# Kernel optimization log

Hardware: AMD Instinct MI355X
Metric: run time of the kernel (lower is better)

Reference implementation:

```python
import jax, jax.numpy as jnp
import numpy as np

N = 50000      # nodes
E = 250000     # edges
D = 256        # in_channels
MSG = 256      # msg_dim
TD = 64        # time encoder out_channels
ED = MSG + TD  # edge_dim = 320
H = 4          # heads
C = 64         # out_channels // heads


def setup_inputs() -> dict:
    key = jax.random.key(0)
    ks = jax.random.split(key, 16)
    s_d = 1.0 / np.sqrt(D)
    s_e = 1.0 / np.sqrt(ED)
    return {
        "x": jax.random.normal(ks[0], (N, D), jnp.float32),
        "last_update": jax.random.uniform(ks[1], (N,), jnp.float32) * 1000.0,
        "t": jax.random.uniform(ks[2], (E,), jnp.float32) * 1000.0,
        "msg": jax.random.normal(ks[3], (E, MSG), jnp.float32),
        "edge_index": jax.random.randint(ks[4], (2, E), 0, N, jnp.int32),
        # TimeEncoder: Linear(1, TD) followed by cos
        "time_w": jax.random.normal(ks[5], (TD,), jnp.float32),
        "time_b": jax.random.normal(ks[6], (TD,), jnp.float32) * 0.1,
        # TransformerConv linears (weights stored [out, in] like torch)
        "Wq": jax.random.normal(ks[7], (H * C, D), jnp.float32) * s_d,
        "bq": jnp.zeros((H * C,), jnp.float32),
        "Wk": jax.random.normal(ks[8], (H * C, D), jnp.float32) * s_d,
        "bk": jnp.zeros((H * C,), jnp.float32),
        "Wv": jax.random.normal(ks[9], (H * C, D), jnp.float32) * s_d,
        "bv": jnp.zeros((H * C,), jnp.float32),
        "We": jax.random.normal(ks[10], (H * C, ED), jnp.float32) * s_e,  # lin_edge, no bias
        "Wskip": jax.random.normal(ks[11], (H * C, D), jnp.float32) * s_d,
        "bskip": jnp.zeros((H * C,), jnp.float32),
    }


def reference(x, last_update, t, msg, edge_index, time_w, time_b,
              Wq, bq, Wk, bk, Wv, bv, We, Wskip, bskip):
    src = edge_index[0]  # j: message source
    dst = edge_index[1]  # i: message target

    # time encoding: cos(Linear(1, TD)(rel_t))
    rel_t = last_update[src] - t                              # [E]
    rel_t_enc = jnp.cos(rel_t[:, None] * time_w[None, :] + time_b)  # [E, TD]
    edge_attr = jnp.concatenate([rel_t_enc, msg], axis=-1)    # [E, ED]

    # TransformerConv (heads=4, concat=True, root_weight=True, beta=False, eval mode)
    q = (x @ Wq.T + bq).reshape(N, H, C)
    k = (x @ Wk.T + bk).reshape(N, H, C)
    v = (x @ Wv.T + bv).reshape(N, H, C)
    e = (edge_attr @ We.T).reshape(E, H, C)

    k_j = k[src] + e                                           # [E, H, C]
    alpha = jnp.einsum('ehc,ehc->eh', q[dst], k_j) / np.sqrt(C)  # [E, H]

    # segment softmax over incoming edges of each target node
    m = jax.ops.segment_max(alpha, dst, num_segments=N)        # [N, H]
    m = jnp.where(jnp.isfinite(m), m, 0.0)
    ex = jnp.exp(alpha - m[dst])                               # [E, H]
    denom = jax.ops.segment_sum(ex, dst, num_segments=N)       # [N, H]
    alpha = ex / (denom[dst] + 1e-16)                          # [E, H]

    out_e = (v[src] + e) * alpha[:, :, None]                   # [E, H, C]
    out = jax.ops.segment_sum(out_e, dst, num_segments=N)      # [N, H, C]
    out = out.reshape(N, H * C) + (x @ Wskip.T + bskip)        # skip connection
    return out
```

## Files before the change

kernel.cpp:

```cpp
#include <hip/hip_runtime.h>
#include <math.h>

#define NN 50000
#define EE 250000

typedef float f32x4 __attribute__((ext_vector_type(4)));
typedef __bf16 bf16x8 __attribute__((ext_vector_type(8)));

static __device__ __forceinline__ ushort f2b(float f) {
    __bf16 h = (__bf16)f;
    return *(ushort*)&h;
}
static __device__ __forceinline__ float b2f(ushort u) {
    return __uint_as_float(((unsigned)u) << 16);
}

__global__ void k_prep_w(const float* __restrict__ Wq, const float* __restrict__ bq,
                         const float* __restrict__ Wk, const float* __restrict__ bk,
                         const float* __restrict__ Wv, const float* __restrict__ bv,
                         const float* __restrict__ Wskip, const float* __restrict__ bskip,
                         const float* __restrict__ We,
                         ushort* __restrict__ Wnb, ushort* __restrict__ Web,
                         float* __restrict__ bcat) {
    int i = blockIdx.x * 256 + threadIdx.x;
    int st = gridDim.x * 256;
    for (int idx = i; idx < 1024 * 256; idx += st) {
        int n = idx >> 8, kk = idx & 255;
        int sel = n >> 8, o = n & 255;
        const float* W = (sel == 0) ? Wq : (sel == 1) ? Wk : (sel == 2) ? Wv : Wskip;
        Wnb[idx] = f2b(W[o * 256 + kk]);
    }
    for (int idx = i; idx < 256 * 320; idx += st) Web[idx] = f2b(We[idx]);
    for (int idx = i; idx < 1024; idx += st) {
        int sel = idx >> 8, o = idx & 255;
        const float* b = (sel == 0) ? bq : (sel == 1) ? bk : (sel == 2) ? bv : bskip;
        bcat[idx] = b[o];
    }
}

__global__ void k_zero(unsigned* __restrict__ deg) {
    int i = blockIdx.x * 256 + threadIdx.x;
    if (i < NN) deg[i] = 0u;
}

__global__ void k_hist(const int* __restrict__ ei, unsigned* __restrict__ deg) {
    int i = blockIdx.x * 256 + threadIdx.x;
    if (i < EE) atomicAdd(&deg[ei[EE + i]], 1u);
}

__global__ __launch_bounds__(1024) void k_scan(const unsigned* __restrict__ deg,
                                               unsigned* __restrict__ offs,
                                               unsigned* __restrict__ cursor) {
    __shared__ unsigned part[1024];
    int t = threadIdx.x;
    const int CH = (NN + 1023) / 1024;
    int b0 = t * CH;
    unsigned s = 0;
    for (int i = 0; i < CH; ++i) { int idx = b0 + i; if (idx < NN) s += deg[idx]; }
    part[t] = s;
    __syncthreads();
    for (int d = 1; d < 1024; d <<= 1) {
        unsigned v = (t >= d) ? part[t - d] : 0u;
        __syncthreads();
        part[t] += v;
        __syncthreads();
    }
    unsigned run = (t == 0) ? 0u : part[t - 1];
    for (int i = 0; i < CH; ++i) {
        int idx = b0 + i;
        if (idx < NN) { offs[idx] = run; cursor[idx] = run; run += deg[idx]; }
    }
    if (t == 1023) offs[NN] = EE;
}

__global__ void k_scatter(const int* __restrict__ ei, unsigned* __restrict__ cursor,
                          int* __restrict__ rank) {
    int i = blockIdx.x * 256 + threadIdx.x;
    if (i < EE) {
        unsigned p = atomicAdd(&cursor[ei[EE + i]], 1u);
        rank[i] = (int)p;
    }
}

__global__ __launch_bounds__(256) void k_node_mfma(
        const float* __restrict__ x, const ushort* __restrict__ Wnb,
        const float* __restrict__ bcat,
        ushort* __restrict__ qb, ushort* __restrict__ kb, ushort* __restrict__ vb,
        float* __restrict__ out) {
    __shared__ ushort As[128 * 64];
    __shared__ ushort Bs[128 * 64];
    int tid = threadIdx.x;
    int lane = tid & 63, wid = tid >> 6;
    int wr = wid >> 1, wc = wid & 1;
    int li = lane & 15, g = lane >> 4;
    int bm = blockIdx.x, bn = blockIdx.y;
    f32x4 acc[4][4] = {};
    for (int k0 = 0; k0 < 256; k0 += 64) {
        __syncthreads();
        #pragma unroll
        for (int i = 0; i < 4; ++i) {
            int ch = tid + i * 256;
            int r = ch >> 3, c = ch & 7;
            int row = bm * 128 + r;
            union { ushort u[8]; uint4 v; } s;
            if (row < NN) {
                const float* xr = x + (size_t)row * 256 + k0 + c * 8;
                float4 a = *(const float4*)xr;
                float4 b = *(const float4*)(xr + 4);
                s.u[0] = f2b(a.x); s.u[1] = f2b(a.y); s.u[2] = f2b(a.z); s.u[3] = f2b(a.w);
                s.u[4] = f2b(b.x); s.u[5] = f2b(b.y); s.u[6] = f2b(b.z); s.u[7] = f2b(b.w);
            } else {
                s.v = make_uint4(0, 0, 0, 0);
            }
            *(uint4*)&As[r * 64 + ((c ^ (r & 7)) * 8)] = s.v;
            uint4 vb4 = *(const uint4*)(Wnb + (size_t)(bn * 128 + r) * 256 + k0 + c * 8);
            *(uint4*)&Bs[r * 64 + ((c ^ (r & 7)) * 8)] = vb4;
        }
        __syncthreads();
        #pragma unroll
        for (int kk = 0; kk < 2; ++kk) {
            bf16x8 a[4], b[4];
            #pragma unroll
            for (int m = 0; m < 4; ++m) {
                int r = wr * 64 + m * 16 + li;
                a[m] = *(const bf16x8*)&As[r * 64 + (((kk * 4 + g) ^ (r & 7)) * 8)];
            }
            #pragma unroll
            for (int n = 0; n < 4; ++n) {
                int r = wc * 64 + n * 16 + li;
                b[n] = *(const bf16x8*)&Bs[r * 64 + (((kk * 4 + g) ^ (r & 7)) * 8)];
            }
            #pragma unroll
            for (int m = 0; m < 4; ++m)
                #pragma unroll
                for (int n = 0; n < 4; ++n)
                    acc[m][n] = __builtin_amdgcn_mfma_f32_16x16x32_bf16(a[m], b[n], acc[m][n], 0, 0, 0);
        }
    }
    int sel = bn >> 1;
    int cbase = (bn & 1) * 128;
    ushort* dstb = (sel == 0) ? qb : (sel == 1) ? kb : vb;
    #pragma unroll
    for (int m = 0; m < 4; ++m) {
        #pragma unroll
        for (int r = 0; r < 4; ++r) {
            int row = bm * 128 + wr * 64 + m * 16 + g * 4 + r;
            if (row >= NN) continue;
            #pragma unroll
            for (int n = 0; n < 4; ++n) {
                int coll = wc * 64 + n * 16 + li;
                float val = acc[m][n][r] + bcat[bn * 128 + coll];
                int cin = cbase + coll;
                if (sel < 3) dstb[(size_t)row * 256 + cin] = f2b(val);
                else         out[(size_t)row * 256 + cin] = val;
            }
        }
    }
}

__global__ __launch_bounds__(256) void k_edge_mfma(
        const float* __restrict__ msg, const float* __restrict__ t_arr,
        const float* __restrict__ lu, const float* __restrict__ tw,
        const float* __restrict__ tb, const ushort* __restrict__ Web,
        const ushort* __restrict__ qb, const ushort* __restrict__ kb,
        const ushort* __restrict__ vb, const int* __restrict__ ei,
        const int* __restrict__ rank,
        ushort* __restrict__ ebuf, float* __restrict__ alpha) {
    __shared__ ushort SS[64 * 328];
    __shared__ int s_src[64], s_dst[64], s_rank[64];
    __shared__ float s_relt[64];
    int tid = threadIdx.x;
    int lane = tid & 63, wid = tid >> 6;
    int wr = wid >> 1, wc = wid & 1;
    int li = lane & 15, g = lane >> 4;
    int e0 = blockIdx.x * 64;
    if (tid < 64) {
        int e = e0 + tid;
        if (e >= EE) e = EE - 1;
        int s = ei[e];
        s_src[tid] = s;
        s_dst[tid] = ei[EE + e];
        s_rank[tid] = rank[e];
        s_relt[tid] = lu[s] - t_arr[e];
    }
    f32x4 acc[2][8] = {};
    for (int k0 = 0; k0 < 320; k0 += 64) {
        __syncthreads();
        #pragma unroll
        for (int i = 0; i < 2; ++i) {
            int ch = tid + i * 256;
            int r = ch >> 3, c = ch & 7;
            union { ushort u[8]; uint4 v; } s;
            if (k0 == 0) {
                float rt = s_relt[r];
                #pragma unroll
                for (int j = 0; j < 8; ++j)
                    s.u[j] = f2b(cosf(rt * tw[c * 8 + j] + tb[c * 8 + j]));
            } else {
                int erow = e0 + r; if (erow >= EE) erow = EE - 1;
                const float* mrow = msg + (size_t)erow * 256 + (k0 - 64) + c * 8;
                float4 a = *(const float4*)mrow;
                float4 b = *(const float4*)(mrow + 4);
                s.u[0] = f2b(a.x); s.u[1] = f2b(a.y); s.u[2] = f2b(a.z); s.u[3] = f2b(a.w);
                s.u[4] = f2b(b.x); s.u[5] = f2b(b.y); s.u[6] = f2b(b.z); s.u[7] = f2b(b.w);
            }
            *(uint4*)&SS[r * 64 + ((c ^ (r & 7)) * 8)] = s.v;
        }
        #pragma unroll
        for (int i = 0; i < 8; ++i) {
            int ch = tid + i * 256;
            int r = ch >> 3, c = ch & 7;
            uint4 vb4 = *(const uint4*)(Web + (size_t)r * 320 + k0 + c * 8);
            *(uint4*)&SS[4096 + r * 64 + ((c ^ (r & 7)) * 8)] = vb4;
        }
        __syncthreads();
        #pragma unroll
        for (int kk = 0; kk < 2; ++kk) {
            bf16x8 a[2], b[8];
            #pragma unroll
            for (int m = 0; m < 2; ++m) {
                int r = wr * 32 + m * 16 + li;
                a[m] = *(const bf16x8*)&SS[r * 64 + (((kk * 4 + g) ^ (r & 7)) * 8)];
            }
            #pragma unroll
            for (int n = 0; n < 8; ++n) {
                int r = wc * 128 + n * 16 + li;
                b[n] = *(const bf16x8*)&SS[4096 + r * 64 + (((kk * 4 + g) ^ (r & 7)) * 8)];
            }
            #pragma unroll
            for (int m = 0; m < 2; ++m)
                #pragma unroll
                for (int n = 0; n < 8; ++n)
                    acc[m][n] = __builtin_amdgcn_mfma_f32_16x16x32_bf16(a[m], b[n], acc[m][n], 0, 0, 0);
        }
    }
    __syncthreads();
    #pragma unroll
    for (int i = 0; i < 8; ++i) {
        int idx = tid + i * 256;
        int r = idx >> 5, c = idx & 31;
        uint4 vv = *(const uint4*)(vb + (size_t)s_src[r] * 256 + c * 8);
        *(uint4*)&SS[r * 328 + c * 8] = vv;
    }
    __syncthreads();
    #pragma unroll
    for (int m = 0; m < 2; ++m) {
        #pragma unroll
        for (int r = 0; r < 4; ++r) {
            int el = wr * 32 + m * 16 + g * 4 + r;
            int edge = e0 + el;
            if (edge >= EE) continue;
            size_t rb = (size_t)s_rank[el] * 256;
            #pragma unroll
            for (int n = 0; n < 8; ++n) {
                int col = wc * 128 + n * 16 + li;
                ebuf[rb + col] = f2b(acc[m][n][r] + b2f(SS[el * 328 + col]));
            }
        }
    }
    __syncthreads();
    #pragma unroll
    for (int i = 0; i < 8; ++i) {
        int idx = tid + i * 256;
        int r = idx >> 5, c = idx & 31;
        uint4 kv = *(const uint4*)(kb + (size_t)s_src[r] * 256 + c * 8);
        *(uint4*)&SS[r * 328 + c * 8] = kv;
    }
    __syncthreads();
    #pragma unroll
    for (int m = 0; m < 2; ++m)
        #pragma unroll
        for (int r = 0; r < 4; ++r) {
            int el = wr * 32 + m * 16 + g * 4 + r;
            #pragma unroll
            for (int n = 0; n < 8; ++n)
                acc[m][n][r] += b2f(SS[el * 328 + wc * 128 + n * 16 + li]);
        }
    __syncthreads();
    #pragma unroll
    for (int i = 0; i < 8; ++i) {
        int idx = tid + i * 256;
        int r = idx >> 5, c = idx & 31;
        uint4 qv = *(const uint4*)(qb + (size_t)s_dst[r] * 256 + c * 8);
        *(uint4*)&SS[r * 328 + c * 8] = qv;
    }
    __syncthreads();
    #pragma unroll
    for (int m = 0; m < 2; ++m) {
        #pragma unroll
        for (int r = 0; r < 4; ++r) {
            int el = wr * 32 + m * 16 + g * 4 + r;
            int edge = e0 + el;
            float p0 = 0.f, p1 = 0.f;
            #pragma unroll
            for (int n = 0; n < 8; ++n) {
                float qv = b2f(SS[el * 328 + wc * 128 + n * 16 + li]);
                float tt = qv * acc[m][n][r];
                if (n < 4) p0 += tt; else p1 += tt;
            }
            #pragma unroll
            for (int msk = 1; msk < 16; msk <<= 1) {
                p0 += __shfl_xor(p0, msk);
                p1 += __shfl_xor(p1, msk);
            }
            if (li < 2 && edge < EE) {
                float av = ((li == 0) ? p0 : p1) * 0.125f;
                int h = wc * 2 + li;
                alpha[(size_t)s_rank[el] * 4 + h] = av;
            }
        }
    }
}

__global__ __launch_bounds__(256) void k_gather(
        const ushort* __restrict__ ebuf, const float* __restrict__ alpha,
        const unsigned* __restrict__ offs, float* __restrict__ out) {
    int wid = threadIdx.x >> 6, lane = threadIdx.x & 63;
    int n = blockIdx.x * 4 + wid;
    if (n >= NN) return;
    unsigned p0 = offs[n], p1 = offs[n + 1];
    if (p0 == p1) return;
    int h = lane >> 4;
    int c0 = lane * 4;
    float m = -INFINITY;
    for (unsigned p = p0; p < p1; ++p)
        m = fmaxf(m, alpha[(size_t)p * 4 + h]);
    f32x4 acc = {0.f, 0.f, 0.f, 0.f};
    float denom = 0.f;
    for (unsigned p = p0; p < p1; ++p) {
        float ex = __expf(alpha[(size_t)p * 4 + h] - m);
        ushort4 ev = *(const ushort4*)(ebuf + (size_t)p * 256 + c0);
        acc[0] += b2f(ev.x) * ex;
        acc[1] += b2f(ev.y) * ex;
        acc[2] += b2f(ev.z) * ex;
        acc[3] += b2f(ev.w) * ex;
        denom += ex;
    }
    float inv = 1.f / (denom + 1e-16f);
    float4 o = *(float4*)(out + (size_t)n * 256 + c0);
    o.x += acc[0] * inv;
    o.y += acc[1] * inv;
    o.z += acc[2] * inv;
    o.w += acc[3] * inv;
    *(float4*)(out + (size_t)n * 256 + c0) = o;
}

extern "C" void kernel_launch(void* const* d_in, const int* in_sizes, int n_in,
                              void* d_out, int out_size, void* d_ws, size_t ws_size,
                              hipStream_t stream) {
    const float* x        = (const float*)d_in[0];
    const float* last_upd = (const float*)d_in[1];
    const float* t_arr    = (const float*)d_in[2];
    const float* msg      = (const float*)d_in[3];
    const int*   ei       = (const int*)d_in[4];
    const float* time_w   = (const float*)d_in[5];
    const float* time_b   = (const float*)d_in[6];
    const float* Wq = (const float*)d_in[7];  const float* bq = (const float*)d_in[8];
    const float* Wk = (const float*)d_in[9];  const float* bk = (const float*)d_in[10];
    const float* Wv = (const float*)d_in[11]; const float* bv = (const float*)d_in[12];
    const float* We = (const float*)d_in[13];
    const float* Wsk = (const float*)d_in[14]; const float* bsk = (const float*)d_in[15];
    float* out = (float*)d_out;
    char* base = (char*)d_ws;

    size_t off = 0;
    auto carve = [&](size_t bytes) {
        void* p = base + off;
        off += (bytes + 255) & ~(size_t)255;
        return p;
    };
    ushort* Wnb   = (ushort*)carve((size_t)1024 * 256 * 2);
    ushort* Web   = (ushort*)carve((size_t)256 * 320 * 2);
    float*  bcat  = (float*) carve(1024 * 4);
    ushort* qb    = (ushort*)carve((size_t)NN * 256 * 2);
    ushort* kb    = (ushort*)carve((size_t)NN * 256 * 2);
    ushort* vb    = (ushort*)carve((size_t)NN * 256 * 2);
    ushort* ebuf  = (ushort*)carve((size_t)EE * 256 * 2);
    float*  alpha = (float*) carve((size_t)EE * 4 * 4);
    unsigned* deg    = (unsigned*)carve((size_t)NN * 4);
    unsigned* cursor = (unsigned*)carve((size_t)NN * 4);
    unsigned* offs   = (unsigned*)carve((size_t)(NN + 1) * 4);
    int*      rank   = (int*)     carve((size_t)EE * 4);

    k_prep_w<<<dim3(512), dim3(256), 0, stream>>>(Wq, bq, Wk, bk, Wv, bv, Wsk, bsk, We,
                                                  Wnb, Web, bcat);
    k_zero<<<dim3((NN + 255) / 256), dim3(256), 0, stream>>>(deg);
    k_hist<<<dim3((EE + 255) / 256), dim3(256), 0, stream>>>(ei, deg);
    k_scan<<<dim3(1), dim3(1024), 0, stream>>>(deg, offs, cursor);
    k_scatter<<<dim3((EE + 255) / 256), dim3(256), 0, stream>>>(ei, cursor, rank);
    k_node_mfma<<<dim3(391, 8), dim3(256), 0, stream>>>(x, Wnb, bcat, qb, kb, vb, out);
    k_edge_mfma<<<dim3((EE + 63) / 64), dim3(256), 0, stream>>>(
        msg, t_arr, last_upd, time_w, time_b, Web, qb, kb, vb, ei, rank, ebuf, alpha);
    k_gather<<<dim3((NN + 3) / 4), dim3(256), 0, stream>>>(ebuf, alpha, offs, out);
}
```

Measured before the change: 584.4 us.

## Shrink edge-kernel LDS footprint to raise occupancy with half-tile epilogue

The edge MFMA kernel now uses a K-step of 32 instead of 64 with padded, unswizzled tiles, and processes the v/k/q gather epilogue in two 32-edge halves. This cuts shared memory from about 42KB to 25.6KB, and __launch_bounds__(256,4) asks the compiler for four resident blocks per CU. The goal is more overlap of the latency-bound gathers. The cost is twice as many K-loop barriers and an epilogue where half the waves sit idle in each phase.

```diff
diff --git a/kernel.cpp b/kernel.cpp
--- a/kernel.cpp
+++ b/kernel.cpp
@@ -158,7 +158,7 @@
     }
 }
 
-__global__ __launch_bounds__(256) void k_edge_mfma(
+__global__ __launch_bounds__(256, 4) void k_edge_mfma(
         const float* __restrict__ msg, const float* __restrict__ t_arr,
         const float* __restrict__ lu, const float* __restrict__ tw,
         const float* __restrict__ tb, const ushort* __restrict__ Web,
@@ -166,7 +166,7 @@
         const ushort* __restrict__ vb, const int* __restrict__ ei,
         const int* __restrict__ rank,
         ushort* __restrict__ ebuf, float* __restrict__ alpha) {
-    __shared__ ushort SS[64 * 328];
+    __shared__ ushort SS[12800];
     __shared__ int s_src[64], s_dst[64], s_rank[64];
     __shared__ float s_relt[64];
     int tid = threadIdx.x;
@@ -184,18 +184,16 @@
         s_relt[tid] = lu[s] - t_arr[e];
     }
     f32x4 acc[2][8] = {};
-    for (int k0 = 0; k0 < 320; k0 += 64) {
-        __syncthreads();
-        #pragma unroll
-        for (int i = 0; i < 2; ++i) {
-            int ch = tid + i * 256;
-            int r = ch >> 3, c = ch & 7;
+    for (int k0 = 0; k0 < 320; k0 += 32) {
+        __syncthreads();
+        {
+            int r = tid >> 2, c = tid & 3;
             union { ushort u[8]; uint4 v; } s;
-            if (k0 == 0) {
+            if (k0 < 64) {
                 float rt = s_relt[r];
                 #pragma unroll
                 for (int j = 0; j < 8; ++j)
-                    s.u[j] = f2b(cosf(rt * tw[c * 8 + j] + tb[c * 8 + j]));
+                    s.u[j] = f2b(cosf(rt * tw[k0 + c * 8 + j] + tb[k0 + c * 8 + j]));
             } else {
                 int erow = e0 + r; if (erow >= EE) erow = EE - 1;
                 const float* mrow = msg + (size_t)erow * 256 + (k0 - 64) + c * 8;
@@ -204,109 +202,112 @@
                 s.u[0] = f2b(a.x); s.u[1] = f2b(a.y); s.u[2] = f2b(a.z); s.u[3] = f2b(a.w);
                 s.u[4] = f2b(b.x); s.u[5] = f2b(b.y); s.u[6] = f2b(b.z); s.u[7] = f2b(b.w);
             }
-            *(uint4*)&SS[r * 64 + ((c ^ (r & 7)) * 8)] = s.v;
-        }
-        #pragma unroll
-        for (int i = 0; i < 8; ++i) {
-            int ch = tid + i * 256;
-            int r = ch >> 3, c = ch & 7;
-            uint4 vb4 = *(const uint4*)(Web + (size_t)r * 320 + k0 + c * 8);
-            *(uint4*)&SS[4096 + r * 64 + ((c ^ (r & 7)) * 8)] = vb4;
-        }
-        __syncthreads();
-        #pragma unroll
-        for (int kk = 0; kk < 2; ++kk) {
-            bf16x8 a[2], b[8];
+            *(uint4*)&SS[r * 40 + c * 8] = s.v;
+        }
+        #pragma unroll
+        for (int i = 0; i < 4; ++i) {
+            int ch = tid + i * 256;
+            int r = ch >> 2, c = ch & 3;
+            uint4 w = *(const uint4*)(Web + (size_t)r * 320 + k0 + c * 8);
+            *(uint4*)&SS[2560 + r * 40 + c * 8] = w;
+        }
+        __syncthreads();
+        bf16x8 a[2], b[8];
+        #pragma unroll
+        for (int m = 0; m < 2; ++m)
+            a[m] = *(const bf16x8*)&SS[(wr * 32 + m * 16 + li) * 40 + g * 8];
+        #pragma unroll
+        for (int n = 0; n < 8; ++n)
+            b[n] = *(const bf16x8*)&SS[2560 + (wc * 128 + n * 16 + li) * 40 + g * 8];
+        #pragma unroll
+        for (int m = 0; m < 2; ++m)
+            #pragma unroll
+            for (int n = 0; n < 8; ++n)
+                acc[m][n] = __builtin_amdgcn_mfma_f32_16x16x32_bf16(a[m], b[n], acc[m][n], 0, 0, 0);
+    }
+    #pragma unroll
+    for (int hh = 0; hh < 2; ++hh) {
+        bool own = (wr == hh);
+        __syncthreads();
+        #pragma unroll
+        for (int i = 0; i < 4; ++i) {
+            int ch = tid + i * 256;
+            int r = ch >> 5, c = ch & 31;
+            uint4 vv = *(const uint4*)(vb + (size_t)s_src[hh * 32 + r] * 256 + c * 8);
+            *(uint4*)&SS[r * 264 + c * 8] = vv;
+        }
+        __syncthreads();
+        if (own) {
             #pragma unroll
             for (int m = 0; m < 2; ++m) {
-                int r = wr * 32 + m * 16 + li;
-                a[m] = *(const bf16x8*)&SS[r * 64 + (((kk * 4 + g) ^ (r & 7)) * 8)];
-            }
-            #pragma unroll
-            for (int n = 0; n < 8; ++n) {
-                int r = wc * 128 + n * 16 + li;
-                b[n] = *(const bf16x8*)&SS[4096 + r * 64 + (((kk * 4 + g) ^ (r & 7)) * 8)];
-            }
+                #pragma unroll
+                for (int r = 0; r < 4; ++r) {
+                    int el = m * 16 + g * 4 + r;
+                    int edge = e0 + hh * 32 + el;
+                    if (edge >= EE) continue;
+                    size_t rb = (size_t)s_rank[hh * 32 + el] * 256;
+                    #pragma unroll
+                    for (int n = 0; n < 8; ++n) {
+                        int col = wc * 128 + n * 16 + li;
+                        ebuf[rb + col] = f2b(acc[m][n][r] + b2f(SS[el * 264 + col]));
+                    }
+                }
+            }
+        }
+        __syncthreads();
+        #pragma unroll
+        for (int i = 0; i < 4; ++i) {
+            int ch = tid + i * 256;
+            int r = ch >> 5, c = ch & 31;
+            uint4 kv = *(const uint4*)(kb + (size_t)s_src[hh * 32 + r] * 256 + c * 8);
+            *(uint4*)&SS[r * 264 + c * 8] = kv;
+        }
+        __syncthreads();
+        if (own) {
             #pragma unroll
             for (int m = 0; m < 2; ++m)
                 #pragma unroll
-                for (int n = 0; n < 8; ++n)
-                    acc[m][n] = __builtin_amdgcn_mfma_f32_16x16x32_bf16(a[m], b[n], acc[m][n], 0, 0, 0);
-        }
-    }
-    __syncthreads();
-    #pragma unroll
-    for (int i = 0; i < 8; ++i) {
-        int idx = tid + i * 256;
-        int r = idx >> 5, c = idx & 31;
-        uint4 vv = *(const uint4*)(vb + (size_t)s_src[r] * 256 + c * 8);
-        *(uint4*)&SS[r * 328 + c * 8] = vv;
-    }
-    __syncthreads();
-    #pragma unroll
-    for (int m = 0; m < 2; ++m) {
-        #pragma unroll
-        for (int r = 0; r < 4; ++r) {
-            int el = wr * 32 + m * 16 + g * 4 + r;
-            int edge = e0 + el;
-            if (edge >= EE) continue;
-            size_t rb = (size_t)s_rank[el] * 256;
-            #pragma unroll
-            for (int n = 0; n < 8; ++n) {
-                int col = wc * 128 + n * 16 + li;
-                ebuf[rb + col] = f2b(acc[m][n][r] + b2f(SS[el * 328 + col]));
-            }
-        }
-    }
-    __syncthreads();
-    #pragma unroll
-    for (int i = 0; i < 8; ++i) {
-        int idx = tid + i * 256;
-        int r = idx >> 5, c = idx & 31;
-        uint4 kv = *(const uint4*)(kb + (size_t)s_src[r] * 256 + c * 8);
-        *(uint4*)&SS[r * 328 + c * 8] = kv;
-    }
-    __syncthreads();
-    #pragma unroll
-    for (int m = 0; m < 2; ++m)
-        #pragma unroll
-        for (int r = 0; r < 4; ++r) {
-            int el = wr * 32 + m * 16 + g * 4 + r;
-            #pragma unroll
-            for (int n = 0; n < 8; ++n)
-                acc[m][n][r] += b2f(SS[el * 328 + wc * 128 + n * 16 + li]);
-        }
-    __syncthreads();
-    #pragma unroll
-    for (int i = 0; i < 8; ++i) {
-        int idx = tid + i * 256;
-        int r = idx >> 5, c = idx & 31;
-        uint4 qv = *(const uint4*)(qb + (size_t)s_dst[r] * 256 + c * 8);
-        *(uint4*)&SS[r * 328 + c * 8] = qv;
-    }
-    __syncthreads();
-    #pragma unroll
-    for (int m = 0; m < 2; ++m) {
-        #pragma unroll
-        for (int r = 0; r < 4; ++r) {
-            int el = wr * 32 + m * 16 + g * 4 + r;
-            int edge = e0 + el;
-            float p0 = 0.f, p1 = 0.f;
-            #pragma unroll
-            for (int n = 0; n < 8; ++n) {
-                float qv = b2f(SS[el * 328 + wc * 128 + n * 16 + li]);
-                float tt = qv * acc[m][n][r];
-                if (n < 4) p0 += tt; else p1 += tt;
-            }
-            #pragma unroll
-            for (int msk = 1; msk < 16; msk <<= 1) {
-                p0 += __shfl_xor(p0, msk);
-                p1 += __shfl_xor(p1, msk);
-            }
-            if (li < 2 && edge < EE) {
-                float av = ((li == 0) ? p0 : p1) * 0.125f;
-                int h = wc * 2 + li;
-                alpha[(size_t)s_rank[el] * 4 + h] = av;
+                for (int r = 0; r < 4; ++r) {
+                    int el = m * 16 + g * 4 + r;
+                    #pragma unroll
+                    for (int n = 0; n < 8; ++n)
+                        acc[m][n][r] += b2f(SS[el * 264 + wc * 128 + n * 16 + li]);
+                }
+        }
+        __syncthreads();
+        #pragma unroll
+        for (int i = 0; i < 4; ++i) {
+            int ch = tid + i * 256;
+            int r = ch >> 5, c = ch & 31;
+            uint4 qv = *(const uint4*)(qb + (size_t)s_dst[hh * 32 + r] * 256 + c * 8);
+            *(uint4*)&SS[r * 264 + c * 8] = qv;
+        }
+        __syncthreads();
+        if (own) {
+            #pragma unroll
+            for (int m = 0; m < 2; ++m) {
+                #pragma unroll
+                for (int r = 0; r < 4; ++r) {
+                    int el = m * 16 + g * 4 + r;
+                    int edge = e0 + hh * 32 + el;
+                    float p0 = 0.f, p1 = 0.f;
+                    #pragma unroll
+                    for (int n = 0; n < 8; ++n) {
+                        float qv = b2f(SS[el * 264 + wc * 128 + n * 16 + li]);
+                        float tt = qv * acc[m][n][r];
+                        if (n < 4) p0 += tt; else p1 += tt;
+                    }
+                    #pragma unroll
+                    for (int msk = 1; msk < 16; msk <<= 1) {
+                        p0 += __shfl_xor(p0, msk);
+                        p1 += __shfl_xor(p1, msk);
+                    }
+                    if (li < 2 && edge < EE) {
+                        float av = ((li == 0) ? p0 : p1) * 0.125f;
+                        int h = wc * 2 + li;
+                        alpha[(size_t)s_rank[hh * 32 + el] * 4 + h] = av;
+                    }
+                }
             }
         }
     }
```

Result: slower. 606.4 us (+3.8%).

## Keep full-K x tile resident in LDS and loop over weight column blocks

Applied to the files above, without the earlier changes.

The node projection GEMM now loads a 64-row x tile with full K=256 into shared memory once, converting fp32 to bf16 a single time. It then loops over 8 weight column blocks of 64, so each block covers 512 of the 1024 output columns, where before every (row, column-block) tile re-read and re-converted x. This cuts redundant global reads and conversions of x, at the cost of smaller 2x2 MFMA tiles per wave, more LDS (64 KB) and more syncs per block.

```diff
diff --git a/kernel.cpp b/kernel.cpp
--- a/kernel.cpp
+++ b/kernel.cpp
@@ -87,72 +87,83 @@
         const float* __restrict__ bcat,
         ushort* __restrict__ qb, ushort* __restrict__ kb, ushort* __restrict__ vb,
         float* __restrict__ out) {
-    __shared__ ushort As[128 * 64];
-    __shared__ ushort Bs[128 * 64];
+    __shared__ ushort As[64 * 256];
+    __shared__ ushort Bs[64 * 256];
     int tid = threadIdx.x;
     int lane = tid & 63, wid = tid >> 6;
-    int wr = wid >> 1, wc = wid & 1;
+    int wrow = wid >> 1, wcol = wid & 1;
     int li = lane & 15, g = lane >> 4;
-    int bm = blockIdx.x, bn = blockIdx.y;
-    f32x4 acc[4][4] = {};
-    for (int k0 = 0; k0 < 256; k0 += 64) {
-        __syncthreads();
-        #pragma unroll
-        for (int i = 0; i < 4; ++i) {
+    int bm = blockIdx.x, bng = blockIdx.y;
+    #pragma unroll
+    for (int i = 0; i < 8; ++i) {
+        int ch = tid + i * 256;
+        int r = ch >> 5, c = ch & 31;
+        int row = bm * 64 + r;
+        union { ushort u[8]; uint4 v; } s;
+        if (row < NN) {
+            const float* xr = x + (size_t)row * 256 + c * 8;
+            float4 a = *(const float4*)xr;
+            float4 b = *(const float4*)(xr + 4);
+            s.u[0] = f2b(a.x); s.u[1] = f2b(a.y); s.u[2] = f2b(a.z); s.u[3] = f2b(a.w);
+            s.u[4] = f2b(b.x); s.u[5] = f2b(b.y); s.u[6] = f2b(b.z); s.u[7] = f2b(b.w);
+        } else {
+            s.v = make_uint4(0, 0, 0, 0);
+        }
+        int sc = (c & 24) | ((c ^ r) & 7);
+        *(uint4*)&As[r * 256 + sc * 8] = s.v;
+    }
+    for (int bn = 0; bn < 8; ++bn) {
+        int bng2 = bng * 8 + bn;
+        __syncthreads();
+        #pragma unroll
+        for (int i = 0; i < 8; ++i) {
             int ch = tid + i * 256;
-            int r = ch >> 3, c = ch & 7;
-            int row = bm * 128 + r;
-            union { ushort u[8]; uint4 v; } s;
-            if (row < NN) {
-                const float* xr = x + (size_t)row * 256 + k0 + c * 8;
-                float4 a = *(const float4*)xr;
-                float4 b = *(const float4*)(xr + 4);
-                s.u[0] = f2b(a.x); s.u[1] = f2b(a.y); s.u[2] = f2b(a.z); s.u[3] = f2b(a.w);
-                s.u[4] = f2b(b.x); s.u[5] = f2b(b.y); s.u[6] = f2b(b.z); s.u[7] = f2b(b.w);
-            } else {
-                s.v = make_uint4(0, 0, 0, 0);
-            }
-            *(uint4*)&As[r * 64 + ((c ^ (r & 7)) * 8)] = s.v;
-            uint4 vb4 = *(const uint4*)(Wnb + (size_t)(bn * 128 + r) * 256 + k0 + c * 8);
-            *(uint4*)&Bs[r * 64 + ((c ^ (r & 7)) * 8)] = vb4;
-        }
-        __syncthreads();
-        #pragma unroll
-        for (int kk = 0; kk < 2; ++kk) {
-            bf16x8 a[4], b[4];
-            #pragma unroll
-            for (int m = 0; m < 4; ++m) {
-                int r = wr * 64 + m * 16 + li;
-                a[m] = *(const bf16x8*)&As[r * 64 + (((kk * 4 + g) ^ (r & 7)) * 8)];
-            }
-            #pragma unroll
-            for (int n = 0; n < 4; ++n) {
-                int r = wc * 64 + n * 16 + li;
-                b[n] = *(const bf16x8*)&Bs[r * 64 + (((kk * 4 + g) ^ (r & 7)) * 8)];
-            }
-            #pragma unroll
-            for (int m = 0; m < 4; ++m)
+            int r = ch >> 5, c = ch & 31;
+            uint4 w = *(const uint4*)(Wnb + (size_t)(bng2 * 64 + r) * 256 + c * 8);
+            int sc = (c & 24) | ((c ^ r) & 7);
+            *(uint4*)&Bs[r * 256 + sc * 8] = w;
+        }
+        __syncthreads();
+        f32x4 acc[2][2] = {};
+        #pragma unroll
+        for (int ks = 0; ks < 8; ++ks) {
+            bf16x8 a[2], b[2];
+            int c = ks * 4 + g;
+            #pragma unroll
+            for (int m = 0; m < 2; ++m) {
+                int r = wrow * 32 + m * 16 + li;
+                int sc = (c & 24) | ((c ^ r) & 7);
+                a[m] = *(const bf16x8*)&As[r * 256 + sc * 8];
+            }
+            #pragma unroll
+            for (int n = 0; n < 2; ++n) {
+                int r = wcol * 32 + n * 16 + li;
+                int sc = (c & 24) | ((c ^ r) & 7);
+                b[n] = *(const bf16x8*)&Bs[r * 256 + sc * 8];
+            }
+            #pragma unroll
+            for (int m = 0; m < 2; ++m)
                 #pragma unroll
-                for (int n = 0; n < 4; ++n)
+                for (int n = 0; n < 2; ++n)
                     acc[m][n] = __builtin_amdgcn_mfma_f32_16x16x32_bf16(a[m], b[n], acc[m][n], 0, 0, 0);
         }
-    }
-    int sel = bn >> 1;
-    int cbase = (bn & 1) * 128;
-    ushort* dstb = (sel == 0) ? qb : (sel == 1) ? kb : vb;
-    #pragma unroll
-    for (int m = 0; m < 4; ++m) {
-        #pragma unroll
-        for (int r = 0; r < 4; ++r) {
-            int row = bm * 128 + wr * 64 + m * 16 + g * 4 + r;
-            if (row >= NN) continue;
-            #pragma unroll
-            for (int n = 0; n < 4; ++n) {
-                int coll = wc * 64 + n * 16 + li;
-                float val = acc[m][n][r] + bcat[bn * 128 + coll];
-                int cin = cbase + coll;
-                if (sel < 3) dstb[(size_t)row * 256 + cin] = f2b(val);
-                else         out[(size_t)row * 256 + cin] = val;
+        int sel = bng2 >> 2;
+        int cbase = (bng2 & 3) * 64;
+        ushort* dstb = (sel == 0) ? qb : (sel == 1) ? kb : vb;
+        #pragma unroll
+        for (int m = 0; m < 2; ++m) {
+            #pragma unroll
+            for (int r = 0; r < 4; ++r) {
+                int row = bm * 64 + wrow * 32 + m * 16 + g * 4 + r;
+                if (row >= NN) continue;
+                #pragma unroll
+                for (int n = 0; n < 2; ++n) {
+                    int coll = wcol * 32 + n * 16 + li;
+                    float val = acc[m][n][r] + bcat[bng2 * 64 + coll];
+                    int cin = cbase + coll;
+                    if (sel < 3) dstb[(size_t)row * 256 + cin] = f2b(val);
+                    else         out[(size_t)row * 256 + cin] = val;
+                }
             }
         }
     }
@@ -388,7 +399,7 @@
     k_hist<<<dim3((EE + 255) / 256), dim3(256), 0, stream>>>(ei, deg);
     k_scan<<<dim3(1), dim3(1024), 0, stream>>>(deg, offs, cursor);
     k_scatter<<<dim3((EE + 255) / 256), dim3(256), 0, stream>>>(ei, cursor, rank);
-    k_node_mfma<<<dim3(391, 8), dim3(256), 0, stream>>>(x, Wnb, bcat, qb, kb, vb, out);
+    k_node_mfma<<<dim3(782, 2), dim3(256), 0, stream>>>(x, Wnb, bcat, qb, kb, vb, out);
     k_edge_mfma<<<dim3((EE + 63) / 64), dim3(256), 0, stream>>>(
         msg, t_arr, last_upd, time_w, time_b, Web, qb, kb, vb, ei, rank, ebuf, alpha);
     k_gather<<<dim3((NN + 3) / 4), dim3(256), 0, stream>>>(ebuf, alpha, offs, out);
```

Measured after the change: 562.1 us. 3.8% less time.
